# Optimization experiments

Hardware: AMD Instinct MI355X
Metric: run time of the kernel (lower is better)

## Reference

```python
import jax, jax.numpy as jnp
import numpy as np

N_HEADS = 16
N_KV_HEADS = 8
N_REP = 2
HEAD_DIM = 128
SOFTCAP = 50.0
NEG_INF = -2.3819763e38
ROPE_BASE = 10000.0


def _rotate_half(x):
    x1, x2 = jnp.split(x, 2, axis=-1)
    return jnp.concatenate((-x2, x1), axis=-1)


def _rope_cos_sin(seq_len, dtype):
    # Gemma2RotaryEmbedding: inv_freq over even dims, emb = cat(freqs, freqs)
    inv_freq = 1.0 / (ROPE_BASE ** (jnp.arange(0, HEAD_DIM, 2, dtype=jnp.float32) / HEAD_DIM))
    freqs = jnp.arange(seq_len, dtype=jnp.float32)[:, None] * inv_freq[None, :]  # [s, hd/2]
    emb = jnp.concatenate((freqs, freqs), axis=-1)  # [s, hd]
    return jnp.cos(emb).astype(dtype), jnp.sin(emb).astype(dtype)


def setup_inputs() -> dict:
    key = jax.random.key(0)
    ks = jax.random.split(key, 5)
    b, s, d = 2, 2048, 2048
    w_scale = 0.02
    return {
        "x": jax.random.normal(ks[0], (b, s, d), dtype=jnp.float32),
        "wq": jax.random.normal(ks[1], (N_HEADS * HEAD_DIM, d), dtype=jnp.float32) * w_scale,
        "wk": jax.random.normal(ks[2], (N_KV_HEADS * HEAD_DIM, d), dtype=jnp.float32) * w_scale,
        "wv": jax.random.normal(ks[3], (N_KV_HEADS * HEAD_DIM, d), dtype=jnp.float32) * w_scale,
        "wo": jax.random.normal(ks[4], (d, N_HEADS * HEAD_DIM), dtype=jnp.float32) * w_scale,
    }


def reference(x, wq, wk, wv, wo):
    b, s, d = x.shape
    # QKV projections (linear_fn = plain x @ W.T)
    xq = (x @ wq.T).reshape(b, s, N_HEADS, HEAD_DIM).transpose(0, 2, 1, 3)      # [b,h,s,hd]
    xk = (x @ wk.T).reshape(b, s, N_KV_HEADS, HEAD_DIM).transpose(0, 2, 1, 3)   # [b,kv,s,hd]
    xv = (x @ wv.T).reshape(b, s, N_KV_HEADS, HEAD_DIM).transpose(0, 2, 1, 3)
    # Gemma2 rotary on q, k
    cos, sin = _rope_cos_sin(s, x.dtype)  # [s,hd] each, broadcast over b,h
    xq = xq * cos + _rotate_half(xq) * sin
    xk = xk * cos + _rotate_half(xk) * sin
    # repeat_kv: expand kv heads to n_heads
    keys = jnp.repeat(xk, N_REP, axis=1)
    values = jnp.repeat(xv, N_REP, axis=1)
    # scores with scaling and Gemma2 logit softcapping
    scale = float(HEAD_DIM) ** -0.5
    scores = jnp.einsum("bhsd,bhtd->bhst", xq * scale, keys)
    scores = jnp.tanh(scores / SOFTCAP) * SOFTCAP
    # causal additive mask [s, t]
    q_pos = jnp.arange(s)[:, None]
    k_pos = jnp.arange(s)[None, :]
    mask = jnp.where(k_pos <= q_pos, 0.0, NEG_INF).astype(jnp.float32)
    scores = scores + mask  # broadcast over [b,h]
    probs = jax.nn.softmax(scores.astype(jnp.float32), axis=-1).astype(xq.dtype)
    out = jnp.einsum("bhst,bhtd->bhsd", probs, values)
    out = out.transpose(0, 2, 1, 3).reshape(b, s, N_HEADS * HEAD_DIM)
    return out @ wo.T
```

## Files before the change

kernel.cpp:

```cpp
#include <hip/hip_runtime.h>
#include <stdint.h>
#include <stddef.h>

#define S_LEN   2048
#define DMODEL  2048
#define NHEADS  16
#define NKVH    8
#define HD      128
#define QPRE 0.0051006994f
#define C1 72.13475204444817f
#define C2 144.26950408889634f

typedef __attribute__((ext_vector_type(8))) short  short8;
typedef __attribute__((ext_vector_type(4))) float  float4v;

static __device__ __forceinline__ unsigned short f2bf(float f) {
  union { float f; unsigned int u; } v; v.f = f;
  unsigned int u = v.u;
  u += 0x7fffu + ((u >> 16) & 1u);
  return (unsigned short)(u >> 16);
}
static __device__ __forceinline__ float bf2f(unsigned short b) {
  union { unsigned int u; float f; } v; v.u = ((unsigned int)b) << 16;
  return v.f;
}
static __device__ __forceinline__ void gload_lds16(const void* g, void* l) {
  __builtin_amdgcn_global_load_lds(
      (const __attribute__((address_space(1))) void*)g,
      (__attribute__((address_space(3))) void*)l, 16, 0, 0);
}

__global__ __launch_bounds__(256) void cvt_f32_to_bf16(
    const float* __restrict__ src, unsigned short* __restrict__ dst, int n4) {
  int i = blockIdx.x * 256 + threadIdx.x;
  if (i >= n4) return;
  float4 v = ((const float4*)src)[i];
  ushort4 o;
  o.x = f2bf(v.x); o.y = f2bf(v.y); o.z = f2bf(v.z); o.w = f2bf(v.w);
  ((ushort4*)dst)[i] = o;
}

__global__ __launch_bounds__(256, 2) void gemm_bf16(
    const unsigned short* __restrict__ A,
    const unsigned short* __restrict__ B,
    void* __restrict__ Cout, int N, int mode) {
  const int t    = threadIdx.x;
  const int lane = t & 63;
  const int w    = t >> 6;
  const int l15  = lane & 15;
  const int quad = lane >> 4;
  const int m0   = blockIdx.y * 128;
  const int n0   = blockIdx.x * 128;
  const int wm   = (w >> 1) * 64;
  const int wn   = (w & 1) * 64;

  __shared__ unsigned short At[128 * 32];
  __shared__ unsigned short Bt[128 * 32];

  float4v acc[4][4];
#pragma unroll
  for (int mt = 0; mt < 4; ++mt)
#pragma unroll
    for (int nt = 0; nt < 4; ++nt)
      acc[mt][nt] = (float4v){0.f, 0.f, 0.f, 0.f};

  const unsigned short* Abase = A + (size_t)m0 * DMODEL;
  const unsigned short* Bbase = B + (size_t)n0 * DMODEL;
  const int srow = w * 16 + (lane >> 2);
  const int sch  = (lane & 3) * 8;

  for (int k0 = 0; k0 < DMODEL; k0 += 32) {
#pragma unroll
    for (int r = 0; r < 2; ++r) {
      gload_lds16(Abase + (size_t)(r * 64 + srow) * DMODEL + k0 + sch,
                  At + (r * 256 + w * 64) * 8);
      gload_lds16(Bbase + (size_t)(r * 64 + srow) * DMODEL + k0 + sch,
                  Bt + (r * 256 + w * 64) * 8);
    }
    __syncthreads();
    short8 af[4], bf[4];
#pragma unroll
    for (int mt = 0; mt < 4; ++mt)
      af[mt] = *(const short8*)(At + (wm + mt * 16 + l15) * 32 + quad * 8);
#pragma unroll
    for (int nt = 0; nt < 4; ++nt)
      bf[nt] = *(const short8*)(Bt + (wn + nt * 16 + l15) * 32 + quad * 8);
#pragma unroll
    for (int mt = 0; mt < 4; ++mt)
#pragma unroll
      for (int nt = 0; nt < 4; ++nt)
        acc[mt][nt] = __builtin_amdgcn_mfma_f32_16x16x32_bf16(
            af[mt], bf[nt], acc[mt][nt], 0, 0, 0);
    __syncthreads();
  }

  if (mode == 2) {
    float* C = (float*)Cout;
#pragma unroll
    for (int mt = 0; mt < 4; ++mt) {
      int row = m0 + wm + mt * 16 + quad * 4;
#pragma unroll
      for (int nt = 0; nt < 4; ++nt) {
        int col = n0 + wn + nt * 16 + l15;
#pragma unroll
        for (int r2 = 0; r2 < 4; ++r2)
          C[(size_t)(row + r2) * N + col] = acc[mt][nt][r2];
      }
    }
  } else {
    unsigned short* C = (unsigned short*)Cout;
#pragma unroll
    for (int mt = 0; mt < 4; ++mt) {
      int row0 = m0 + wm + mt * 16 + quad * 4;
      int b = row0 >> 11, s0 = row0 & (S_LEN - 1);
#pragma unroll
      for (int nt = 0; nt < 4; ++nt) {
        int col = n0 + wn + nt * 16 + l15;
        if (col < 2048) {
          int head = col >> 7, d = col & (HD - 1);
#pragma unroll
          for (int r2 = 0; r2 < 4; ++r2)
            C[((size_t)(b * 16 + head) * S_LEN + s0 + r2) * HD + d] =
                f2bf(acc[mt][nt][r2]);
        } else if (col < 3072) {
          int c2 = col - 2048;
          int kvh = c2 >> 7, d = c2 & (HD - 1);
#pragma unroll
          for (int r2 = 0; r2 < 4; ++r2)
            C[8388608 + ((size_t)(b * 8 + kvh) * S_LEN + s0 + r2) * HD + d] =
                f2bf(acc[mt][nt][r2]);
        } else {
          int c2 = col - 3072;
          int kvh = c2 >> 7, d = c2 & (HD - 1);
          ushort4 pk;
          pk.x = f2bf(acc[mt][nt][0]); pk.y = f2bf(acc[mt][nt][1]);
          pk.z = f2bf(acc[mt][nt][2]); pk.w = f2bf(acc[mt][nt][3]);
          *(ushort4*)&C[12582912 + ((size_t)(b * 8 + kvh) * HD + d) * S_LEN + s0] = pk;
        }
      }
    }
  }
}

__global__ __launch_bounds__(256) void rope_kernel(unsigned short* __restrict__ Q,
                                                   unsigned short* __restrict__ Kc) {
  int gt = blockIdx.x * 256 + threadIdx.x;
  int r = gt >> 6;
  int j = gt & 63;
  const int QROWS = 2 * NHEADS * S_LEN;
  bool isQ = (r < QROWS);
  unsigned short* p = isQ ? (Q + (size_t)r * HD)
                          : (Kc + (size_t)(r - QROWS) * HD);
  int pos = r & (S_LEN - 1);
  float inv = exp2f(-(float)j * 0.20762050593046868f);
  float ang = (float)pos * inv;
  float c = cosf(ang), s = sinf(ang);
  float sc = isQ ? QPRE : 1.0f;
  float x1 = bf2f(p[j]), x2 = bf2f(p[j + 64]);
  p[j]      = f2bf((x1 * c - x2 * s) * sc);
  p[j + 64] = f2bf((x2 * c + x1 * s) * sc);
}

__global__ __launch_bounds__(128, 2) void attn_kernel(
    const unsigned short* __restrict__ Q,
    const unsigned short* __restrict__ Kc,
    const unsigned short* __restrict__ Vt,
    unsigned short* __restrict__ Aout) {
  const int t    = threadIdx.x;
  const int lane = t & 63;
  const int w    = t >> 6;
  const int l15  = lane & 15;
  const int quad = lane >> 4;
  const int bh = blockIdx.x;
  const int qt = blockIdx.y;
  const int b = bh >> 4, h = bh & 15, kv = h >> 1;
  const int q0 = qt * 64;

  __shared__ unsigned short Ktile[64 * 128];
  __shared__ unsigned short Vtile[128 * 64];
  __shared__ unsigned short Ptile[2 * 32 * 64];

  int offK[8], offV[8];
#pragma unroll
  for (int i = 0; i < 8; ++i) {
    int g = i * 128 + t;
    int rK = g >> 4, cK = (g & 15) ^ (rK & 7);
    offK[i] = rK * HD + cK * 8;
    int rV = g >> 3, cV = (g & 7) ^ (rV & 7);
    offV[i] = rV * S_LEN + cV * 8;
  }

  const unsigned short* Qb = Q + ((size_t)(b * NHEADS + h) * S_LEN + q0 + w * 32) * HD;
  short8 qf[2][4];
#pragma unroll
  for (int ntq = 0; ntq < 2; ++ntq)
#pragma unroll
    for (int kk = 0; kk < 4; ++kk)
      qf[ntq][kk] = *(const short8*)&Qb[(ntq * 16 + l15) * HD + kk * 32 + quad * 8];

  float4v o[2][8];
#pragma unroll
  for (int ntq = 0; ntq < 2; ++ntq)
#pragma unroll
    for (int nth = 0; nth < 8; ++nth)
      o[ntq][nth] = (float4v){0.f, 0.f, 0.f, 0.f};
  float lsum[2] = {0.f, 0.f};

  const unsigned short* kg = Kc + (size_t)(b * NKVH + kv) * S_LEN * HD;
  const unsigned short* vg = Vt + (size_t)(b * NKVH + kv) * HD * S_LEN;
  unsigned short* Pw = Ptile + w * 2048;

  for (int kt = 0; kt <= qt; ++kt) {
#pragma unroll
    for (int i = 0; i < 8; ++i)
      gload_lds16(kg + offK[i], Ktile + (i * 128 + w * 64) * 8);
#pragma unroll
    for (int i = 0; i < 8; ++i)
      gload_lds16(vg + offV[i], Vtile + (i * 128 + w * 64) * 8);
    __syncthreads();

    const bool diag = (kt == qt);
#pragma unroll
    for (int ntk = 0; ntk < 4; ++ntk) {
      int pb = l15 * 64 + (((ntk * 2 + (quad >> 1)) ^ (l15 & 7)) * 8) + (quad & 1) * 4;
      if (diag && (ntk * 16 > w * 32 + 31)) {
        uint2 z; z.x = 0u; z.y = 0u;
        *(uint2*)&Pw[pb] = z;
        *(uint2*)&Pw[pb + 1024] = z;
        continue;
      }
      short8 kf[4];
#pragma unroll
      for (int kk = 0; kk < 4; ++kk)
        kf[kk] = *(const short8*)
            &Ktile[(ntk * 16 + l15) * HD + (((kk * 4 + quad) ^ (l15 & 7)) * 8)];
      float4v s[2];
      s[0] = (float4v){0.f, 0.f, 0.f, 0.f};
      s[1] = s[0];
#pragma unroll
      for (int kk = 0; kk < 4; ++kk) {
        s[0] = __builtin_amdgcn_mfma_f32_16x16x32_bf16(kf[kk], qf[0][kk], s[0], 0, 0, 0);
        s[1] = __builtin_amdgcn_mfma_f32_16x16x32_bf16(kf[kk], qf[1][kk], s[1], 0, 0, 0);
      }
#pragma unroll
      for (int ntq = 0; ntq < 2; ++ntq) {
        float pv[4];
#pragma unroll
        for (int r = 0; r < 4; ++r) {
          float e2 = __builtin_amdgcn_exp2f(s[ntq][r]);
          float rc = __builtin_amdgcn_rcpf(e2 + 1.f);
          float p = __builtin_amdgcn_exp2f(C1 - C2 * rc);
          if (diag)
            p = (ntk * 16 + quad * 4 + r <= w * 32 + ntq * 16 + l15) ? p : 0.f;
          lsum[ntq] += p;
          pv[r] = p;
        }
        union { float f; unsigned u; } u0, u1, u2, u3;
        u0.f = pv[0]; u1.f = pv[1]; u2.f = pv[2]; u3.f = pv[3];
        uint2 pk;
        pk.x = __builtin_amdgcn_perm(u1.u, u0.u, 0x07060302);
        pk.y = __builtin_amdgcn_perm(u3.u, u2.u, 0x07060302);
        *(uint2*)&Pw[pb + ntq * 1024] = pk;
      }
    }

#pragma unroll
    for (int kk = 0; kk < 2; ++kk) {
      int sw = ((kk * 4 + quad) ^ (l15 & 7)) * 8;
      short8 pf0 = *(const short8*)&Pw[l15 * 64 + sw];
      short8 pf1 = *(const short8*)&Pw[(16 + l15) * 64 + sw];
#pragma unroll
      for (int nth = 0; nth < 8; ++nth) {
        short8 vf = *(const short8*)&Vtile[(nth * 16 + l15) * 64 + sw];
        o[0][nth] = __builtin_amdgcn_mfma_f32_16x16x32_bf16(pf0, vf, o[0][nth], 0, 0, 0);
        o[1][nth] = __builtin_amdgcn_mfma_f32_16x16x32_bf16(pf1, vf, o[1][nth], 0, 0, 0);
      }
    }
    __syncthreads();
    kg += 64 * HD;
    vg += 64;
  }

  float inv[2];
#pragma unroll
  for (int ntq = 0; ntq < 2; ++ntq) {
    float v = lsum[ntq];
    v += __shfl_xor(v, 16, 64);
    v += __shfl_xor(v, 32, 64);
    inv[ntq] = __builtin_amdgcn_rcpf(v);
  }
  unsigned short* ob = Aout + (size_t)(b * S_LEN + q0 + w * 32) * DMODEL + h * HD;
#pragma unroll
  for (int ntq = 0; ntq < 2; ++ntq) {
    float iv[4];
#pragma unroll
    for (int r = 0; r < 4; ++r) iv[r] = __shfl(inv[ntq], quad * 4 + r, 64);
#pragma unroll
    for (int nth = 0; nth < 8; ++nth) {
#pragma unroll
      for (int r = 0; r < 4; ++r) {
        int row = ntq * 16 + quad * 4 + r;
        ob[(size_t)row * DMODEL + nth * 16 + l15] = f2bf(o[ntq][nth][r] * iv[r]);
      }
    }
  }
}

extern "C" void kernel_launch(void* const* d_in, const int* in_sizes, int n_in,
                              void* d_out, int out_size, void* d_ws, size_t ws_size,
                              hipStream_t stream) {
  const float* x  = (const float*)d_in[0];
  const float* wq = (const float*)d_in[1];
  const float* wk = (const float*)d_in[2];
  const float* wv = (const float*)d_in[3];
  const float* wo = (const float*)d_in[4];

  char* ws = (char*)d_ws;
  unsigned short* xb   = (unsigned short*)(ws + 0);
  unsigned short* wcat = (unsigned short*)(ws + 16777216);
  unsigned short* wob  = (unsigned short*)(ws + 33554432);
  unsigned short* QKV  = (unsigned short*)(ws + 41943040);
  unsigned short* AO   = (unsigned short*)(ws + 75497472);

  unsigned short* Qw = QKV;
  unsigned short* Kw = QKV + 8388608;
  unsigned short* Vw = QKV + 12582912;

  cvt_f32_to_bf16<<<8192, 256, 0, stream>>>(x,  xb,  2097152);
  cvt_f32_to_bf16<<<4096, 256, 0, stream>>>(wq, wcat,           1048576);
  cvt_f32_to_bf16<<<2048, 256, 0, stream>>>(wk, wcat + 4194304,  524288);
  cvt_f32_to_bf16<<<2048, 256, 0, stream>>>(wv, wcat + 6291456,  524288);
  cvt_f32_to_bf16<<<4096, 256, 0, stream>>>(wo, wob, 1048576);

  gemm_bf16<<<dim3(32, 32), 256, 0, stream>>>(xb, wcat, QKV, 4096, 3);

  rope_kernel<<<24576, 256, 0, stream>>>(Qw, Kw);

  attn_kernel<<<dim3(32, 32), 128, 0, stream>>>(Qw, Kw, Vw, AO);

  gemm_bf16<<<dim3(16, 32), 256, 0, stream>>>(AO, wob, d_out, 2048, 2);
}
```

Baseline: 362.2 us.

## Pair causal query tiles per block, double-buffer K/V, fuse conversion kernels

Each attention block now handles two query tiles, pp and 31-pp, so every block does about the same causal work, and the two tiles share each staged K/V tile. K/V loads are double-buffered: the next tile is prefetched while the current one is computed, and the trailing barrier is dropped. The five fp32-to-bf16 conversion launches are merged into one kernel. This doubles accumulator register use and LDS per block and removes the occupancy hint of 2, which may lower occupancy or cause spills.

```diff
diff --git a/kernel.cpp b/kernel.cpp
--- a/kernel.cpp
+++ b/kernel.cpp
@@ -30,14 +30,23 @@
       (__attribute__((address_space(3))) void*)l, 16, 0, 0);
 }
 
-__global__ __launch_bounds__(256) void cvt_f32_to_bf16(
-    const float* __restrict__ src, unsigned short* __restrict__ dst, int n4) {
+__global__ __launch_bounds__(256) void cvt_all(
+    const float* __restrict__ x,  const float* __restrict__ wq,
+    const float* __restrict__ wk, const float* __restrict__ wv,
+    const float* __restrict__ wo,
+    ushort4* __restrict__ xb, ushort4* __restrict__ wcat,
+    ushort4* __restrict__ wob) {
   int i = blockIdx.x * 256 + threadIdx.x;
-  if (i >= n4) return;
-  float4 v = ((const float4*)src)[i];
+  const float4* src; ushort4* dst; int j;
+  if (i < 2097152)      { src = (const float4*)x;  dst = xb;             j = i; }
+  else if (i < 3145728) { src = (const float4*)wq; dst = wcat;           j = i - 2097152; }
+  else if (i < 3670016) { src = (const float4*)wk; dst = wcat + 1048576; j = i - 3145728; }
+  else if (i < 4194304) { src = (const float4*)wv; dst = wcat + 1572864; j = i - 3670016; }
+  else                  { src = (const float4*)wo; dst = wob;            j = i - 4194304; }
+  float4 v = src[j];
   ushort4 o;
   o.x = f2bf(v.x); o.y = f2bf(v.y); o.z = f2bf(v.z); o.w = f2bf(v.w);
-  ((ushort4*)dst)[i] = o;
+  dst[j] = o;
 }
 
 __global__ __launch_bounds__(256, 2) void gemm_bf16(
@@ -161,7 +170,7 @@
   p[j + 64] = f2bf((x2 * c + x1 * s) * sc);
 }
 
-__global__ __launch_bounds__(128, 2) void attn_kernel(
+__global__ __launch_bounds__(128) void attn_kernel(
     const unsigned short* __restrict__ Q,
     const unsigned short* __restrict__ Kc,
     const unsigned short* __restrict__ Vt,
@@ -172,13 +181,15 @@
   const int l15  = lane & 15;
   const int quad = lane >> 4;
   const int bh = blockIdx.x;
-  const int qt = blockIdx.y;
+  const int pp = blockIdx.y;
   const int b = bh >> 4, h = bh & 15, kv = h >> 1;
-  const int q0 = qt * 64;
-
-  __shared__ unsigned short Ktile[64 * 128];
-  __shared__ unsigned short Vtile[128 * 64];
-  __shared__ unsigned short Ptile[2 * 32 * 64];
+  const int qtA = pp, qtB = 31 - pp;
+  const int q0A = qtA * 64, q0B = qtB * 64;
+  const int ntB = qtB + 1;
+
+  __shared__ unsigned short Kt[2][64 * 128];
+  __shared__ unsigned short Vts[2][128 * 64];
+  __shared__ unsigned short Pt[2 * 2 * 2048];
 
   int offK[8], offV[8];
 #pragma unroll
@@ -190,117 +201,181 @@
     offV[i] = rV * S_LEN + cV * 8;
   }
 
-  const unsigned short* Qb = Q + ((size_t)(b * NHEADS + h) * S_LEN + q0 + w * 32) * HD;
-  short8 qf[2][4];
+  const unsigned short* QA = Q + ((size_t)(b * NHEADS + h) * S_LEN + q0A + w * 32) * HD;
+  const unsigned short* QB = Q + ((size_t)(b * NHEADS + h) * S_LEN + q0B + w * 32) * HD;
+  short8 qfA[2][4], qfB[2][4];
 #pragma unroll
   for (int ntq = 0; ntq < 2; ++ntq)
 #pragma unroll
-    for (int kk = 0; kk < 4; ++kk)
-      qf[ntq][kk] = *(const short8*)&Qb[(ntq * 16 + l15) * HD + kk * 32 + quad * 8];
-
-  float4v o[2][8];
+    for (int kk = 0; kk < 4; ++kk) {
+      qfA[ntq][kk] = *(const short8*)&QA[(ntq * 16 + l15) * HD + kk * 32 + quad * 8];
+      qfB[ntq][kk] = *(const short8*)&QB[(ntq * 16 + l15) * HD + kk * 32 + quad * 8];
+    }
+
+  float4v oA[2][8], oB[2][8];
 #pragma unroll
   for (int ntq = 0; ntq < 2; ++ntq)
 #pragma unroll
-    for (int nth = 0; nth < 8; ++nth)
-      o[ntq][nth] = (float4v){0.f, 0.f, 0.f, 0.f};
-  float lsum[2] = {0.f, 0.f};
-
-  const unsigned short* kg = Kc + (size_t)(b * NKVH + kv) * S_LEN * HD;
-  const unsigned short* vg = Vt + (size_t)(b * NKVH + kv) * HD * S_LEN;
-  unsigned short* Pw = Ptile + w * 2048;
-
-  for (int kt = 0; kt <= qt; ++kt) {
+    for (int nth = 0; nth < 8; ++nth) {
+      oA[ntq][nth] = (float4v){0.f, 0.f, 0.f, 0.f};
+      oB[ntq][nth] = (float4v){0.f, 0.f, 0.f, 0.f};
+    }
+  float lsA[2] = {0.f, 0.f}, lsB[2] = {0.f, 0.f};
+
+  const unsigned short* kg0 = Kc + (size_t)(b * NKVH + kv) * S_LEN * HD;
+  const unsigned short* vg0 = Vt + (size_t)(b * NKVH + kv) * HD * S_LEN;
+  unsigned short* PB = Pt + (w * 2 + 0) * 2048;
+  unsigned short* PA = Pt + (w * 2 + 1) * 2048;
+
+  auto stage = [&](int buf, int kt) {
+    const unsigned short* kgp = kg0 + (size_t)kt * 64 * HD;
+    const unsigned short* vgp = vg0 + (size_t)kt * 64;
 #pragma unroll
     for (int i = 0; i < 8; ++i)
-      gload_lds16(kg + offK[i], Ktile + (i * 128 + w * 64) * 8);
+      gload_lds16(kgp + offK[i], &Kt[buf][(i * 128 + w * 64) * 8]);
 #pragma unroll
     for (int i = 0; i < 8; ++i)
-      gload_lds16(vg + offV[i], Vtile + (i * 128 + w * 64) * 8);
+      gload_lds16(vgp + offV[i], &Vts[buf][(i * 128 + w * 64) * 8]);
+  };
+
+  stage(0, 0);
+  for (int kt = 0; kt < ntB; ++kt) {
     __syncthreads();
-
-    const bool diag = (kt == qt);
+    if (kt + 1 < ntB) stage((kt + 1) & 1, kt + 1);
+    const int cur = kt & 1;
+    const bool doA   = (kt <= qtA);
+    const bool diagA = (kt == qtA);
+    const bool diagB = (kt == qtB);
+    const unsigned short* Kcur = &Kt[cur][0];
+    const unsigned short* Vcur = &Vts[cur][0];
+
 #pragma unroll
     for (int ntk = 0; ntk < 4; ++ntk) {
       int pb = l15 * 64 + (((ntk * 2 + (quad >> 1)) ^ (l15 & 7)) * 8) + (quad & 1) * 4;
-      if (diag && (ntk * 16 > w * 32 + 31)) {
-        uint2 z; z.x = 0u; z.y = 0u;
-        *(uint2*)&Pw[pb] = z;
-        *(uint2*)&Pw[pb + 1024] = z;
-        continue;
-      }
       short8 kf[4];
 #pragma unroll
       for (int kk = 0; kk < 4; ++kk)
         kf[kk] = *(const short8*)
-            &Ktile[(ntk * 16 + l15) * HD + (((kk * 4 + quad) ^ (l15 & 7)) * 8)];
-      float4v s[2];
-      s[0] = (float4v){0.f, 0.f, 0.f, 0.f};
-      s[1] = s[0];
-#pragma unroll
-      for (int kk = 0; kk < 4; ++kk) {
-        s[0] = __builtin_amdgcn_mfma_f32_16x16x32_bf16(kf[kk], qf[0][kk], s[0], 0, 0, 0);
-        s[1] = __builtin_amdgcn_mfma_f32_16x16x32_bf16(kf[kk], qf[1][kk], s[1], 0, 0, 0);
-      }
-#pragma unroll
-      for (int ntq = 0; ntq < 2; ++ntq) {
-        float pv[4];
-#pragma unroll
-        for (int r = 0; r < 4; ++r) {
-          float e2 = __builtin_amdgcn_exp2f(s[ntq][r]);
-          float rc = __builtin_amdgcn_rcpf(e2 + 1.f);
-          float p = __builtin_amdgcn_exp2f(C1 - C2 * rc);
-          if (diag)
-            p = (ntk * 16 + quad * 4 + r <= w * 32 + ntq * 16 + l15) ? p : 0.f;
-          lsum[ntq] += p;
-          pv[r] = p;
-        }
-        union { float f; unsigned u; } u0, u1, u2, u3;
-        u0.f = pv[0]; u1.f = pv[1]; u2.f = pv[2]; u3.f = pv[3];
-        uint2 pk;
-        pk.x = __builtin_amdgcn_perm(u1.u, u0.u, 0x07060302);
-        pk.y = __builtin_amdgcn_perm(u3.u, u2.u, 0x07060302);
-        *(uint2*)&Pw[pb + ntq * 1024] = pk;
+            &Kcur[(ntk * 16 + l15) * HD + (((kk * 4 + quad) ^ (l15 & 7)) * 8)];
+
+      if (diagB && (ntk * 16 > w * 32 + 31)) {
+        uint2 z; z.x = 0u; z.y = 0u;
+        *(uint2*)&PB[pb] = z; *(uint2*)&PB[pb + 1024] = z;
+      } else {
+        float4v s0 = (float4v){0.f, 0.f, 0.f, 0.f}, s1 = s0;
+#pragma unroll
+        for (int kk = 0; kk < 4; ++kk) {
+          s0 = __builtin_amdgcn_mfma_f32_16x16x32_bf16(kf[kk], qfB[0][kk], s0, 0, 0, 0);
+          s1 = __builtin_amdgcn_mfma_f32_16x16x32_bf16(kf[kk], qfB[1][kk], s1, 0, 0, 0);
+        }
+#pragma unroll
+        for (int ntq = 0; ntq < 2; ++ntq) {
+          const float4v& sv = ntq ? s1 : s0;
+          float pv[4];
+#pragma unroll
+          for (int r = 0; r < 4; ++r) {
+            float e2 = __builtin_amdgcn_exp2f(sv[r]);
+            float rc = __builtin_amdgcn_rcpf(e2 + 1.f);
+            float p = __builtin_amdgcn_exp2f(C1 - C2 * rc);
+            if (diagB)
+              p = (ntk * 16 + quad * 4 + r <= w * 32 + ntq * 16 + l15) ? p : 0.f;
+            lsB[ntq] += p;
+            pv[r] = p;
+          }
+          union { float f; unsigned u; } u0, u1, u2, u3;
+          u0.f = pv[0]; u1.f = pv[1]; u2.f = pv[2]; u3.f = pv[3];
+          uint2 pk;
+          pk.x = __builtin_amdgcn_perm(u1.u, u0.u, 0x07060302);
+          pk.y = __builtin_amdgcn_perm(u3.u, u2.u, 0x07060302);
+          *(uint2*)&PB[pb + ntq * 1024] = pk;
+        }
+      }
+
+      if (doA) {
+        if (diagA && (ntk * 16 > w * 32 + 31)) {
+          uint2 z; z.x = 0u; z.y = 0u;
+          *(uint2*)&PA[pb] = z; *(uint2*)&PA[pb + 1024] = z;
+        } else {
+          float4v s0 = (float4v){0.f, 0.f, 0.f, 0.f}, s1 = s0;
+#pragma unroll
+          for (int kk = 0; kk < 4; ++kk) {
+            s0 = __builtin_amdgcn_mfma_f32_16x16x32_bf16(kf[kk], qfA[0][kk], s0, 0, 0, 0);
+            s1 = __builtin_amdgcn_mfma_f32_16x16x32_bf16(kf[kk], qfA[1][kk], s1, 0, 0, 0);
+          }
+#pragma unroll
+          for (int ntq = 0; ntq < 2; ++ntq) {
+            const float4v& sv = ntq ? s1 : s0;
+            float pv[4];
+#pragma unroll
+            for (int r = 0; r < 4; ++r) {
+              float e2 = __builtin_amdgcn_exp2f(sv[r]);
+              float rc = __builtin_amdgcn_rcpf(e2 + 1.f);
+              float p = __builtin_amdgcn_exp2f(C1 - C2 * rc);
+              if (diagA)
+                p = (ntk * 16 + quad * 4 + r <= w * 32 + ntq * 16 + l15) ? p : 0.f;
+              lsA[ntq] += p;
+              pv[r] = p;
+            }
+            union { float f; unsigned u; } u0, u1, u2, u3;
+            u0.f = pv[0]; u1.f = pv[1]; u2.f = pv[2]; u3.f = pv[3];
+            uint2 pk;
+            pk.x = __builtin_amdgcn_perm(u1.u, u0.u, 0x07060302);
+            pk.y = __builtin_amdgcn_perm(u3.u, u2.u, 0x07060302);
+            *(uint2*)&PA[pb + ntq * 1024] = pk;
+          }
+        }
       }
     }
 
 #pragma unroll
     for (int kk = 0; kk < 2; ++kk) {
       int sw = ((kk * 4 + quad) ^ (l15 & 7)) * 8;
-      short8 pf0 = *(const short8*)&Pw[l15 * 64 + sw];
-      short8 pf1 = *(const short8*)&Pw[(16 + l15) * 64 + sw];
+      short8 pB0 = *(const short8*)&PB[l15 * 64 + sw];
+      short8 pB1 = *(const short8*)&PB[(16 + l15) * 64 + sw];
+      short8 pA0, pA1;
+      if (doA) {
+        pA0 = *(const short8*)&PA[l15 * 64 + sw];
+        pA1 = *(const short8*)&PA[(16 + l15) * 64 + sw];
+      }
 #pragma unroll
       for (int nth = 0; nth < 8; ++nth) {
-        short8 vf = *(const short8*)&Vtile[(nth * 16 + l15) * 64 + sw];
-        o[0][nth] = __builtin_amdgcn_mfma_f32_16x16x32_bf16(pf0, vf, o[0][nth], 0, 0, 0);
-        o[1][nth] = __builtin_amdgcn_mfma_f32_16x16x32_bf16(pf1, vf, o[1][nth], 0, 0, 0);
-      }
-    }
-    __syncthreads();
-    kg += 64 * HD;
-    vg += 64;
+        short8 vf = *(const short8*)&Vcur[(nth * 16 + l15) * 64 + sw];
+        oB[0][nth] = __builtin_amdgcn_mfma_f32_16x16x32_bf16(pB0, vf, oB[0][nth], 0, 0, 0);
+        oB[1][nth] = __builtin_amdgcn_mfma_f32_16x16x32_bf16(pB1, vf, oB[1][nth], 0, 0, 0);
+        if (doA) {
+          oA[0][nth] = __builtin_amdgcn_mfma_f32_16x16x32_bf16(pA0, vf, oA[0][nth], 0, 0, 0);
+          oA[1][nth] = __builtin_amdgcn_mfma_f32_16x16x32_bf16(pA1, vf, oA[1][nth], 0, 0, 0);
+        }
+      }
+    }
   }
 
-  float inv[2];
-#pragma unroll
-  for (int ntq = 0; ntq < 2; ++ntq) {
-    float v = lsum[ntq];
-    v += __shfl_xor(v, 16, 64);
-    v += __shfl_xor(v, 32, 64);
-    inv[ntq] = __builtin_amdgcn_rcpf(v);
-  }
-  unsigned short* ob = Aout + (size_t)(b * S_LEN + q0 + w * 32) * DMODEL + h * HD;
-#pragma unroll
-  for (int ntq = 0; ntq < 2; ++ntq) {
-    float iv[4];
-#pragma unroll
-    for (int r = 0; r < 4; ++r) iv[r] = __shfl(inv[ntq], quad * 4 + r, 64);
-#pragma unroll
-    for (int nth = 0; nth < 8; ++nth) {
-#pragma unroll
-      for (int r = 0; r < 4; ++r) {
-        int row = ntq * 16 + quad * 4 + r;
-        ob[(size_t)row * DMODEL + nth * 16 + l15] = f2bf(o[ntq][nth][r] * iv[r]);
+#pragma unroll
+  for (int tile = 0; tile < 2; ++tile) {
+    float (&ls)[2] = tile ? lsA : lsB;
+    float4v (&oo)[2][8] = tile ? oA : oB;
+    int q0 = tile ? q0A : q0B;
+    float inv[2];
+#pragma unroll
+    for (int ntq = 0; ntq < 2; ++ntq) {
+      float v = ls[ntq];
+      v += __shfl_xor(v, 16, 64);
+      v += __shfl_xor(v, 32, 64);
+      inv[ntq] = __builtin_amdgcn_rcpf(v);
+    }
+    unsigned short* ob = Aout + (size_t)(b * S_LEN + q0 + w * 32) * DMODEL + h * HD;
+#pragma unroll
+    for (int ntq = 0; ntq < 2; ++ntq) {
+      float iv[4];
+#pragma unroll
+      for (int r = 0; r < 4; ++r) iv[r] = __shfl(inv[ntq], quad * 4 + r, 64);
+#pragma unroll
+      for (int nth = 0; nth < 8; ++nth) {
+#pragma unroll
+        for (int r = 0; r < 4; ++r) {
+          int row = ntq * 16 + quad * 4 + r;
+          ob[(size_t)row * DMODEL + nth * 16 + l15] = f2bf(oo[ntq][nth][r] * iv[r]);
+        }
       }
     }
   }
@@ -326,17 +401,14 @@
   unsigned short* Kw = QKV + 8388608;
   unsigned short* Vw = QKV + 12582912;
 
-  cvt_f32_to_bf16<<<8192, 256, 0, stream>>>(x,  xb,  2097152);
-  cvt_f32_to_bf16<<<4096, 256, 0, stream>>>(wq, wcat,           1048576);
-  cvt_f32_to_bf16<<<2048, 256, 0, stream>>>(wk, wcat + 4194304,  524288);
-  cvt_f32_to_bf16<<<2048, 256, 0, stream>>>(wv, wcat + 6291456,  524288);
-  cvt_f32_to_bf16<<<4096, 256, 0, stream>>>(wo, wob, 1048576);
+  cvt_all<<<20480, 256, 0, stream>>>(x, wq, wk, wv, wo,
+                                     (ushort4*)xb, (ushort4*)wcat, (ushort4*)wob);
 
   gemm_bf16<<<dim3(32, 32), 256, 0, stream>>>(xb, wcat, QKV, 4096, 3);
 
   rope_kernel<<<24576, 256, 0, stream>>>(Qw, Kw);
 
-  attn_kernel<<<dim3(32, 32), 128, 0, stream>>>(Qw, Kw, Vw, AO);
+  attn_kernel<<<dim3(32, 16), 128, 0, stream>>>(Qw, Kw, Vw, AO);
 
   gemm_bf16<<<dim3(16, 32), 256, 0, stream>>>(AO, wob, d_out, 2048, 2);
 }
```

New measurement: 361.0 us. No clear change (-0.3%).
